# Optimization experiments

Measured on AMD Instinct MI355X. Metric: run time of the kernel, lower is better.

Reference implementation:

```python
import jax, jax.numpy as jnp
import numpy as np

EPS = 0.001  # additive floor applied after relu, as in the torch code


def setup_inputs() -> dict:
    key = jax.random.key(0)
    kA, kB, kW = jax.random.split(key, 3)
    M, N, C, H, W = 512, 64, 128, 8, 8
    A = jax.random.normal(kA, (M, C, H, W), dtype=jnp.float32)
    B = jax.random.normal(kB, (N, C, H, W), dtype=jnp.float32)
    Wg = jax.random.normal(kW, (C, C), dtype=jnp.float32) * 0.01  # Wg.data.normal_(0.0, 0.01)
    return {"A": A, "B": B, "Wg": Wg}


def reference(A, B, Wg):
    # Faithful vectorization of MIMOcom.get_source_dst_max(A, B, dir=True).
    # Torch loops i,j over HxW: B0 = B[:, i, j, :]; G = B0 @ Wg;
    # combination[m, n, p] = sum_c A[m, p, c] * G[n, c]; running max over (i, j).
    M, C, H, W = A.shape
    N = B.shape[0]
    P = H * W
    Af = jnp.transpose(A, (0, 2, 3, 1)).reshape(M, P, C)  # [M, P, C]
    Bf = jnp.transpose(B, (0, 2, 3, 1)).reshape(N, P, C)  # [N, Q, C]
    G = Bf @ Wg                                           # [N, Q, D]
    scores = jnp.einsum('mpd,nqd->mnpq', Af, G)           # [M, N, P, Q]
    comb_max = scores.max(axis=-1)                        # max over B positions q
    return jax.nn.relu(comb_max) + EPS                    # [M, N, P]
```

## Files before the change

### kernel.cpp

```cpp
#include <hip/hip_runtime.h>
#include <hip/hip_bf16.h>
#include <stdint.h>

typedef __attribute__((ext_vector_type(8))) short bf16x8;
typedef __attribute__((ext_vector_type(4))) float f32x4;
using bf16 = __hip_bfloat16;

static constexpr int Mdim = 512;
static constexpr int Ndim = 64;
static constexpr int Cdim = 128;
static constexpr int Pdim = 64;
static constexpr float EPS_ADD = 0.001f;

#define SB0 __builtin_amdgcn_sched_barrier(0)
#define WAITV(N) asm volatile("s_waitcnt vmcnt(" #N ")" ::: "memory")

__device__ __forceinline__ void gll16(const void* gsrc, void* ldst) {
    const __attribute__((address_space(1))) unsigned int* g =
        (const __attribute__((address_space(1))) unsigned int*)gsrc;
    __attribute__((address_space(3))) unsigned int* l =
        (__attribute__((address_space(3))) unsigned int*)(uintptr_t)ldst;
    __builtin_amdgcn_global_load_lds(g, l, 16, 0, 0);
}

__global__ void prep_A_kernel(const float* __restrict__ A, bf16* __restrict__ Abf) {
    __shared__ float lds[128 * 65];
    const int m = blockIdx.x;
    const int t = threadIdx.x;
    const float* __restrict__ Am = A + (size_t)m * (Cdim * Pdim);

#pragma unroll
    for (int i = 0; i < 8; ++i) {
        int v = t + i * 256;
        int gidx = v * 4;
        int c = gidx >> 6, p = gidx & 63;
        float4 val = *reinterpret_cast<const float4*>(Am + gidx);
        float* dst = &lds[c * 65 + p];
        dst[0] = val.x; dst[1] = val.y; dst[2] = val.z; dst[3] = val.w;
    }
    __syncthreads();

    bf16* __restrict__ dstm = Abf + (size_t)m * (Pdim * Cdim);
#pragma unroll
    for (int i = 0; i < 16; ++i) {
        int pr = t + i * 256;
        int p = pr >> 6;
        int c = (pr & 63) << 1;
        float f0 = lds[c * 65 + p];
        float f1 = lds[(c + 1) * 65 + p];
        union { bf16 h[2]; unsigned u; } pk;
        pk.h[0] = __float2bfloat16(f0);
        pk.h[1] = __float2bfloat16(f1);
        *reinterpret_cast<unsigned*>(dstm + p * Cdim + c) = pk.u;
    }
}

__global__ void prep_G_kernel(const float* __restrict__ B, const float* __restrict__ Wg,
                              bf16* __restrict__ Gbf) {
    __shared__ float ldsB[128 * 65];
    const int n  = blockIdx.x >> 2;
    const int q0 = (blockIdx.x & 3) * 16;
    const int t = threadIdx.x;
    const float* __restrict__ Bn = B + (size_t)n * (Cdim * Pdim);

#pragma unroll
    for (int i = 0; i < 8; ++i) {
        int v = t + i * 256;
        int gidx = v * 4;
        int c = gidx >> 6, q = gidx & 63;
        float4 val = *reinterpret_cast<const float4*>(Bn + gidx);
        float* dst = &ldsB[c * 65 + q];
        dst[0] = val.x; dst[1] = val.y; dst[2] = val.z; dst[3] = val.w;
    }
    __syncthreads();

    const int d  = t & 127;
    const int qb = q0 + (t >> 7) * 8;
    float acc[8] = {0.f, 0.f, 0.f, 0.f, 0.f, 0.f, 0.f, 0.f};
    for (int c = 0; c < 128; ++c) {
        float w = Wg[c * 128 + d];
#pragma unroll
        for (int qi = 0; qi < 8; ++qi)
            acc[qi] = fmaf(ldsB[c * 65 + qb + qi], w, acc[qi]);
    }
#pragma unroll
    for (int qi = 0; qi < 8; ++qi)
        Gbf[(size_t)(n * 64 + qb + qi) * Cdim + d] = __float2bfloat16(acc[qi]);
}

__global__ __launch_bounds__(512, 2)
void gemm_max_kernel(const bf16* __restrict__ Abf, const bf16* __restrict__ Gbf,
                     float* __restrict__ out) {
    __shared__ bf16 sG[4 * 64 * 128];
    __shared__ bf16 sA[3][64 * 128];
    const int tid  = threadIdx.x;
    const int lane = tid & 63;
    const int w    = tid >> 6;
    const int nw = w >> 1, h = w & 1;
    const int rr = lane & 15, g = lane >> 4;
    const int bm = blockIdx.x & 15;
    const int bn = blockIdx.x >> 4;

    const char* Gsrc = (const char*)Gbf + (size_t)bn * 65536;
#pragma unroll
    for (int i = 0; i < 8; ++i) {
        int f = (i * 512 + tid) * 16;
        gll16(Gsrc + f, (char*)sG + f);
    }
    const char* Abase = (const char*)Abf + (size_t)bm * 32 * 16384;
    auto stageA = [&](int s) {
        char* dst = (char*)&sA[s % 3][0];
        const char* src = Abase + (size_t)s * 16384;
#pragma unroll
        for (int i = 0; i < 2; ++i) {
            int f = (i * 512 + tid) * 16;
            int row = f >> 8;
            int inner = (f & 255) ^ ((row & 7) << 4);
            gll16(src + row * 256 + inner, dst + f);
        }
    };
    stageA(0);
    stageA(1);

    WAITV(4); __builtin_amdgcn_s_barrier(); SB0;
    bf16x8 gf[4][4];
    {
        const char* gb = (const char*)sG + nw * 16384 + rr * 256 + g * 16;
#pragma unroll
        for (int qt = 0; qt < 4; ++qt)
#pragma unroll
            for (int ks = 0; ks < 4; ++ks)
                gf[qt][ks] = *reinterpret_cast<const bf16x8*>(gb + qt * 4096 + ks * 64);
    }

    f32x4 acc[4][2];

    auto compute = [&](int s) {
        const char* ab = (const char*)&sA[s % 3][0] + (h * 32 + rr) * 256;
#pragma unroll
        for (int ks = 0; ks < 4; ++ks) {
            const int off = (ks * 64 + g * 16) ^ ((rr & 7) << 4);
            bf16x8 a0 = *reinterpret_cast<const bf16x8*>(ab + off);
            bf16x8 a1 = *reinterpret_cast<const bf16x8*>(ab + 16 * 256 + off);
#pragma unroll
            for (int qt = 0; qt < 4; ++qt) {
                acc[qt][0] = __builtin_amdgcn_mfma_f32_16x16x32_bf16(
                    gf[qt][ks], a0, ks == 0 ? (f32x4){0.f,0.f,0.f,0.f} : acc[qt][0], 0, 0, 0);
                acc[qt][1] = __builtin_amdgcn_mfma_f32_16x16x32_bf16(
                    gf[qt][ks], a1, ks == 0 ? (f32x4){0.f,0.f,0.f,0.f} : acc[qt][1], 0, 0, 0);
            }
        }
    };

    auto epilogue = [&](int s) {
        float* ob = out + (size_t)(bm * 32 + s) * 4096 + (bn * 4 + nw) * 64 + h * 32;
#pragma unroll
        for (int pt = 0; pt < 2; ++pt) {
            float v = acc[0][pt][0];
#pragma unroll
            for (int qt = 0; qt < 4; ++qt)
#pragma unroll
                for (int j = 0; j < 4; ++j)
                    if (qt || j) v = fmaxf(v, acc[qt][pt][j]);
            v = fmaxf(v, __shfl_xor(v, 16));
            v = fmaxf(v, __shfl_xor(v, 32));
            if (g == 0) ob[pt * 16 + rr] = fmaxf(v, 0.f) + EPS_ADD;
        }
    };

    WAITV(2); __builtin_amdgcn_s_barrier(); SB0;
    compute(0); epilogue(0); SB0; stageA(2); SB0;

    for (int s = 1; s <= 29; ++s) {
        WAITV(4); __builtin_amdgcn_s_barrier(); SB0;
        compute(s); epilogue(s); SB0; stageA(s + 2); SB0;
    }

    WAITV(4); __builtin_amdgcn_s_barrier(); SB0;
    compute(30); epilogue(30); SB0;

    WAITV(2); __builtin_amdgcn_s_barrier(); SB0;
    compute(31); epilogue(31);
}

extern "C" void kernel_launch(void* const* d_in, const int* in_sizes, int n_in,
                              void* d_out, int out_size, void* d_ws, size_t ws_size,
                              hipStream_t stream) {
    const float* A  = (const float*)d_in[0];
    const float* B  = (const float*)d_in[1];
    const float* Wg = (const float*)d_in[2];
    float* out = (float*)d_out;

    bf16* Abf = (bf16*)d_ws;
    bf16* Gbf = (bf16*)((char*)d_ws + (size_t)Mdim * Pdim * Cdim * sizeof(bf16));

    prep_A_kernel<<<Mdim, 256, 0, stream>>>(A, Abf);
    prep_G_kernel<<<256, 256, 0, stream>>>(B, Wg, Gbf);
    gemm_max_kernel<<<256, 512, 0, stream>>>(Abf, Gbf, out);
}
```

Measured before the change: 56.31 us.

## Merge prep kernels and split GEMM blocks to 256 threads with direct G loads

Fuses the A-transpose and G-projection prep kernels into a single launch that dispatches on block index, removing one kernel launch and its inter-kernel gap. The GEMM kernel moves to 256-thread blocks covering two n-groups each, doubling the grid to 512 blocks. Each wave now loads its G fragments straight from global memory into registers, so the shared G staging buffer is gone and LDS per block drops. The A-stage issue is moved ahead of the epilogue so the next prefetch starts sooner, with wait counts adjusted to match. The trade-off is that G is now read from global memory per wave instead of shared through LDS.

```diff
diff --git a/kernel.cpp b/kernel.cpp
--- a/kernel.cpp
+++ b/kernel.cpp
@@ -23,75 +23,73 @@
     __builtin_amdgcn_global_load_lds(g, l, 16, 0, 0);
 }
 
-__global__ void prep_A_kernel(const float* __restrict__ A, bf16* __restrict__ Abf) {
+__global__ void prep_kernel(const float* __restrict__ A, const float* __restrict__ B,
+                            const float* __restrict__ Wg,
+                            bf16* __restrict__ Abf, bf16* __restrict__ Gbf) {
     __shared__ float lds[128 * 65];
-    const int m = blockIdx.x;
     const int t = threadIdx.x;
-    const float* __restrict__ Am = A + (size_t)m * (Cdim * Pdim);
 
+    if (blockIdx.x < 512) {
+        const int m = blockIdx.x;
+        const float* __restrict__ Am = A + (size_t)m * (Cdim * Pdim);
 #pragma unroll
-    for (int i = 0; i < 8; ++i) {
-        int v = t + i * 256;
-        int gidx = v * 4;
-        int c = gidx >> 6, p = gidx & 63;
-        float4 val = *reinterpret_cast<const float4*>(Am + gidx);
-        float* dst = &lds[c * 65 + p];
-        dst[0] = val.x; dst[1] = val.y; dst[2] = val.z; dst[3] = val.w;
-    }
-    __syncthreads();
+        for (int i = 0; i < 8; ++i) {
+            int v = t + i * 256;
+            int gidx = v * 4;
+            int c = gidx >> 6, p = gidx & 63;
+            float4 val = *reinterpret_cast<const float4*>(Am + gidx);
+            float* dst = &lds[c * 65 + p];
+            dst[0] = val.x; dst[1] = val.y; dst[2] = val.z; dst[3] = val.w;
+        }
+        __syncthreads();
 
-    bf16* __restrict__ dstm = Abf + (size_t)m * (Pdim * Cdim);
+        bf16* __restrict__ dstm = Abf + (size_t)m * (Pdim * Cdim);
 #pragma unroll
-    for (int i = 0; i < 16; ++i) {
-        int pr = t + i * 256;
-        int p = pr >> 6;
-        int c = (pr & 63) << 1;
-        float f0 = lds[c * 65 + p];
-        float f1 = lds[(c + 1) * 65 + p];
-        union { bf16 h[2]; unsigned u; } pk;
-        pk.h[0] = __float2bfloat16(f0);
-        pk.h[1] = __float2bfloat16(f1);
-        *reinterpret_cast<unsigned*>(dstm + p * Cdim + c) = pk.u;
+        for (int i = 0; i < 16; ++i) {
+            int pr = t + i * 256;
+            int p = pr >> 6;
+            int c = (pr & 63) << 1;
+            float f0 = lds[c * 65 + p];
+            float f1 = lds[(c + 1) * 65 + p];
+            union { bf16 h[2]; unsigned u; } pk;
+            pk.h[0] = __float2bfloat16(f0);
+            pk.h[1] = __float2bfloat16(f1);
+            *reinterpret_cast<unsigned*>(dstm + p * Cdim + c) = pk.u;
+        }
+    } else {
+        const int nb = blockIdx.x - 512;
+        const int n  = nb >> 2;
+        const int q0 = (nb & 3) * 16;
+        const float* __restrict__ Bn = B + (size_t)n * (Cdim * Pdim);
+#pragma unroll
+        for (int i = 0; i < 8; ++i) {
+            int v = t + i * 256;
+            int gidx = v * 4;
+            int c = gidx >> 6, q = gidx & 63;
+            float4 val = *reinterpret_cast<const float4*>(Bn + gidx);
+            float* dst = &lds[c * 65 + q];
+            dst[0] = val.x; dst[1] = val.y; dst[2] = val.z; dst[3] = val.w;
+        }
+        __syncthreads();
+
+        const int d  = t & 127;
+        const int qb = q0 + (t >> 7) * 8;
+        float acc[8] = {0.f, 0.f, 0.f, 0.f, 0.f, 0.f, 0.f, 0.f};
+        for (int c = 0; c < 128; ++c) {
+            float w = Wg[c * 128 + d];
+#pragma unroll
+            for (int qi = 0; qi < 8; ++qi)
+                acc[qi] = fmaf(lds[c * 65 + qb + qi], w, acc[qi]);
+        }
+#pragma unroll
+        for (int qi = 0; qi < 8; ++qi)
+            Gbf[(size_t)(n * 64 + qb + qi) * Cdim + d] = __float2bfloat16(acc[qi]);
     }
 }
 
-__global__ void prep_G_kernel(const float* __restrict__ B, const float* __restrict__ Wg,
-                              bf16* __restrict__ Gbf) {
-    __shared__ float ldsB[128 * 65];
-    const int n  = blockIdx.x >> 2;
-    const int q0 = (blockIdx.x & 3) * 16;
-    const int t = threadIdx.x;
-    const float* __restrict__ Bn = B + (size_t)n * (Cdim * Pdim);
-
-#pragma unroll
-    for (int i = 0; i < 8; ++i) {
-        int v = t + i * 256;
-        int gidx = v * 4;
-        int c = gidx >> 6, q = gidx & 63;
-        float4 val = *reinterpret_cast<const float4*>(Bn + gidx);
-        float* dst = &ldsB[c * 65 + q];
-        dst[0] = val.x; dst[1] = val.y; dst[2] = val.z; dst[3] = val.w;
-    }
-    __syncthreads();
-
-    const int d  = t & 127;
-    const int qb = q0 + (t >> 7) * 8;
-    float acc[8] = {0.f, 0.f, 0.f, 0.f, 0.f, 0.f, 0.f, 0.f};
-    for (int c = 0; c < 128; ++c) {
-        float w = Wg[c * 128 + d];
-#pragma unroll
-        for (int qi = 0; qi < 8; ++qi)
-            acc[qi] = fmaf(ldsB[c * 65 + qb + qi], w, acc[qi]);
-    }
-#pragma unroll
-    for (int qi = 0; qi < 8; ++qi)
-        Gbf[(size_t)(n * 64 + qb + qi) * Cdim + d] = __float2bfloat16(acc[qi]);
-}
-
-__global__ __launch_bounds__(512, 2)
+__global__ __launch_bounds__(256, 3)
 void gemm_max_kernel(const bf16* __restrict__ Abf, const bf16* __restrict__ Gbf,
                      float* __restrict__ out) {
-    __shared__ bf16 sG[4 * 64 * 128];
     __shared__ bf16 sA[3][64 * 128];
     const int tid  = threadIdx.x;
     const int lane = tid & 63;
@@ -101,19 +99,22 @@
     const int bm = blockIdx.x & 15;
     const int bn = blockIdx.x >> 4;
 
-    const char* Gsrc = (const char*)Gbf + (size_t)bn * 65536;
+    const bf16* Gp = Gbf + ((size_t)((bn * 2 + nw) * 64 + rr)) * 128 + g * 8;
+    bf16x8 gf[4][4];
 #pragma unroll
-    for (int i = 0; i < 8; ++i) {
-        int f = (i * 512 + tid) * 16;
-        gll16(Gsrc + f, (char*)sG + f);
-    }
+    for (int qt = 0; qt < 4; ++qt)
+#pragma unroll
+        for (int ks = 0; ks < 4; ++ks)
+            gf[qt][ks] = *reinterpret_cast<const bf16x8*>(Gp + qt * 16 * 128 + ks * 32);
+    asm volatile("" ::: "memory");
+
     const char* Abase = (const char*)Abf + (size_t)bm * 32 * 16384;
     auto stageA = [&](int s) {
         char* dst = (char*)&sA[s % 3][0];
         const char* src = Abase + (size_t)s * 16384;
 #pragma unroll
-        for (int i = 0; i < 2; ++i) {
-            int f = (i * 512 + tid) * 16;
+        for (int i = 0; i < 4; ++i) {
+            int f = (i * 256 + tid) * 16;
             int row = f >> 8;
             int inner = (f & 255) ^ ((row & 7) << 4);
             gll16(src + row * 256 + inner, dst + f);
@@ -121,17 +122,7 @@
     };
     stageA(0);
     stageA(1);
-
-    WAITV(4); __builtin_amdgcn_s_barrier(); SB0;
-    bf16x8 gf[4][4];
-    {
-        const char* gb = (const char*)sG + nw * 16384 + rr * 256 + g * 16;
-#pragma unroll
-        for (int qt = 0; qt < 4; ++qt)
-#pragma unroll
-            for (int ks = 0; ks < 4; ++ks)
-                gf[qt][ks] = *reinterpret_cast<const bf16x8*>(gb + qt * 4096 + ks * 64);
-    }
+    WAITV(8);
 
     f32x4 acc[4][2];
 
@@ -153,7 +144,7 @@
     };
 
     auto epilogue = [&](int s) {
-        float* ob = out + (size_t)(bm * 32 + s) * 4096 + (bn * 4 + nw) * 64 + h * 32;
+        float* ob = out + (size_t)(bm * 32 + s) * 4096 + (bn * 2 + nw) * 64 + h * 32;
 #pragma unroll
         for (int pt = 0; pt < 2; ++pt) {
             float v = acc[0][pt][0];
@@ -168,18 +159,21 @@
         }
     };
 
-    WAITV(2); __builtin_amdgcn_s_barrier(); SB0;
-    compute(0); epilogue(0); SB0; stageA(2); SB0;
+    WAITV(4); __builtin_amdgcn_s_barrier(); SB0;
+    compute(0); SB0; stageA(2); epilogue(0); SB0;
 
-    for (int s = 1; s <= 29; ++s) {
-        WAITV(4); __builtin_amdgcn_s_barrier(); SB0;
-        compute(s); epilogue(s); SB0; stageA(s + 2); SB0;
+    WAITV(6); __builtin_amdgcn_s_barrier(); SB0;
+    compute(1); SB0; stageA(3); epilogue(1); SB0;
+
+    for (int s = 2; s <= 29; ++s) {
+        WAITV(8); __builtin_amdgcn_s_barrier(); SB0;
+        compute(s); SB0; stageA(s + 2); epilogue(s); SB0;
     }
 
-    WAITV(4); __builtin_amdgcn_s_barrier(); SB0;
+    WAITV(8); __builtin_amdgcn_s_barrier(); SB0;
     compute(30); epilogue(30); SB0;
 
-    WAITV(2); __builtin_amdgcn_s_barrier(); SB0;
+    WAITV(4); __builtin_amdgcn_s_barrier(); SB0;
     compute(31); epilogue(31);
 }
 
@@ -194,7 +188,6 @@
     bf16* Abf = (bf16*)d_ws;
     bf16* Gbf = (bf16*)((char*)d_ws + (size_t)Mdim * Pdim * Cdim * sizeof(bf16));
 
-    prep_A_kernel<<<Mdim, 256, 0, stream>>>(A, Abf);
-    prep_G_kernel<<<256, 256, 0, stream>>>(B, Wg, Gbf);
-    gemm_max_kernel<<<256, 512, 0, stream>>>(Abf, Gbf, out);
+    prep_kernel<<<768, 256, 0, stream>>>(A, B, Wg, Abf, Gbf);
+    gemm_max_kernel<<<512, 256, 0, stream>>>(Abf, Gbf, out);
 }
```

Result: faster. 53.69 us (-4.7%).
